# Kernel optimization log

Measured on AMD Instinct MI355X. Metric: run time of the kernel, lower is better.

The kernel has to match this reference:

```python
import jax, jax.numpy as jnp
import numpy as np

SH_C0 = 0.28209479177387814
SH_C1 = 0.4886025119029199
SH_C2 = (1.0925484305920792, -1.0925484305920792, 0.31539156525252005,
         -1.0925484305920792, 0.5462742152960396)
RADIUS = 0.006  # pyramid level k=0: 0.006 * 2**k


def eval_sh2(sh, dirs):
    # sh: [B, N, 16, 9], dirs: [N, 3] -> [B, N, 16]
    x = dirs[None, :, 0, None]
    y = dirs[None, :, 1, None]
    z = dirs[None, :, 2, None]
    xx, yy, zz = x * x, y * y, z * z
    res = (SH_C0 * sh[..., 0]
           - SH_C1 * y * sh[..., 1] + SH_C1 * z * sh[..., 2] - SH_C1 * x * sh[..., 3]
           + SH_C2[0] * (x * y) * sh[..., 4] + SH_C2[1] * (y * z) * sh[..., 5]
           + SH_C2[2] * (2.0 * zz - xx - yy) * sh[..., 6]
           + SH_C2[3] * (x * z) * sh[..., 7] + SH_C2[4] * (xx - yy) * sh[..., 8])
    return res


def setup_inputs() -> dict:
    key = jax.random.key(0)
    ks = jax.random.split(key, 9)
    P, F, H, W, C = 500000, 200000, 768, 768, 72
    features = jax.random.normal(ks[0], (P, C), jnp.float32)
    faces = jax.random.randint(ks[1], (F, 3), 0, P, jnp.int64)
    idx = jax.random.randint(ks[2], (2, H, W, 1), 0, P, jnp.int64)
    idx = jnp.where(jax.random.uniform(ks[3], (2, H, W, 1)) < 0.3, -1, idx)
    p2f = jax.random.randint(ks[4], (2, H, W, 1), 0, F, jnp.int64)
    p2f = jnp.where(jax.random.uniform(ks[5], (2, H, W, 1)) < 0.3, -1, p2f)
    dists = jax.random.uniform(ks[6], (2, H, W, 1), jnp.float32) * (RADIUS * RADIUS)
    bary = jax.random.uniform(ks[7], (2, H, W, 1, 3), jnp.float32)
    bary = bary / jnp.sum(bary, axis=-1, keepdims=True)
    rd = jax.random.normal(ks[8], (3, H, W), jnp.float32)
    rd = rd / jnp.linalg.norm(rd, axis=0, keepdims=True)
    return {"features": features, "frag1_dists": dists, "frag2_bary": bary,
            "ray_dirs": rd, "faces": faces, "frag1_idx": idx,
            "frag2_pix_to_face": p2f}


def reference(features, frag1_dists, frag2_bary, ray_dirs, faces, frag1_idx, frag2_pix_to_face):
    # frag1_idx / frag2_pix_to_face: [2, H, W, 1] (K=1), -1 == empty pixel
    H, W = frag1_idx.shape[1], frag1_idx.shape[2]
    m1 = frag1_idx >= 0
    m2 = frag2_pix_to_face >= 0
    final_mask = jnp.logical_or(m1, m2)            # [2, H, W, 1]
    weights = 1.0 - frag1_dists / (RADIUS * RADIUS)  # [2, H, W, 1]
    # point-rasterizer gather: features[idx] * mask * weights
    feat1 = features[jnp.maximum(frag1_idx, 0)]    # [2, H, W, 1, C]
    feat1 = feat1 * m1[..., None] * weights[..., None]
    feat1 = feat1[:, :, :, 0, :]                   # [2, H, W, C]
    # mesh-rasterizer barycentric interpolation (interpolate_face_attributes)
    tri = faces[jnp.maximum(frag2_pix_to_face, 0)]  # [2, H, W, 1, 3]
    colors = jnp.zeros_like(feat1)[:, :, :, None, :]
    for v in range(3):  # small fixed loop over triangle vertices
        colors = colors + frag2_bary[..., v:v + 1] * features[tri[..., v]]
    colors = colors * m2[..., None]
    colors = colors[:, :, :, 0, :]                 # [2, H, W, C]
    feat = jnp.concatenate([feat1, colors], axis=-1)  # [2, H, W, 144]
    # ray directions: flip along both image axes, then flatten to [H*W, 3]
    dirs = jnp.flip(ray_dirs, axis=(1, 2)).transpose(1, 2, 0).reshape(-1, 3)
    sh = feat.reshape(2, H * W, 16, 9)
    out = eval_sh2(sh, dirs).reshape(2, H, W, 16)
    out_feat_fg = out[0:1]
    out_feat_bg = out[1:2]
    final_mask_fg = final_mask[0:1]
    final_mask_bg = final_mask[1:2]
    return (out_feat_fg, out_feat_bg, final_mask_fg, final_mask_bg)
```

## Files before the change

kernel.cpp:

```cpp
#include <hip/hip_runtime.h>


constexpr float SH_C0 = 0.28209479177387814f;
constexpr float SH_C1 = 0.4886025119029199f;
constexpr float C20 =  1.0925484305920792f;
constexpr float C21 = -1.0925484305920792f;
constexpr float C22 =  0.31539156525252005f;
constexpr float C23 = -1.0925484305920792f;
constexpr float C24 =  0.5462742152960396f;
constexpr float INV_R2 = 1.0f / (0.006f * 0.006f);

__global__ __launch_bounds__(256) void net_tex_kernel8(
    const float* __restrict__ features,
    const float* __restrict__ dists,
    const float* __restrict__ bary,
    const float* __restrict__ rd,
    const int*  __restrict__ faces,
    const int*  __restrict__ f1idx,
    const int*  __restrict__ p2f,
    float* __restrict__ out,
    int HW, int N)
{
    int q = blockIdx.x * blockDim.x + threadIdx.x;
    int p = q >> 3;
    int r = q & 7;
    if (p >= N) return;
    int role = r >> 1;
    int half = r & 1;

    int s  = (p >= HW) ? 1 : 0;
    int hw = p - s * HW;

    float x = rd[HW   - 1 - hw];
    float y = rd[2*HW - 1 - hw];
    float z = rd[3*HW - 1 - hw];
    float xx = x*x, yy = y*y, zz = z*z;
    float c[9];
    c[0] = SH_C0;
    c[1] = -SH_C1 * y;
    c[2] =  SH_C1 * z;
    c[3] = -SH_C1 * x;
    c[4] = C20 * x * y;
    c[5] = C21 * y * z;
    c[6] = C22 * (2.0f*zz - xx - yy);
    c[7] = C23 * x * z;
    c[8] = C24 * (xx - yy);

    int   idx;
    float w;
    bool  valid;
    if (role == 0) {
        int i1 = f1idx[p];
        valid = (i1 >= 0);
        idx = valid ? i1 : 0;
        w = 1.0f - dists[p] * INV_R2;
    } else {
        int f2 = p2f[p];
        valid = (f2 >= 0);
        int fb = (valid ? f2 : 0) * 3;
        idx = faces[fb + (role - 1)];
        w = bary[(size_t)p * 3 + (role - 1)];
    }

    float d[4];
    #pragma unroll
    for (int j = 0; j < 4; j++) d[j] = 0.0f;

    if (valid) {
        const float4* row =
            (const float4*)(features + (size_t)idx * 72) + half * 9;
        #pragma unroll
        for (int ch = 0; ch < 9; ch++) {
            float4 v = row[ch];
            const int e = ch * 4;
            d[(e+0)/9] += c[(e+0)%9] * v.x;
            d[(e+1)/9] += c[(e+1)%9] * v.y;
            d[(e+2)/9] += c[(e+2)%9] * v.z;
            d[(e+3)/9] += c[(e+3)%9] * v.w;
        }
        #pragma unroll
        for (int j = 0; j < 4; j++) d[j] *= w;
    }

    float sum[4];
    #pragma unroll
    for (int j = 0; j < 4; j++) {
        float t = (role == 0) ? 0.0f : d[j];
        t += __shfl_xor(t, 2, 64);
        t += __shfl_xor(t, 4, 64);
        sum[j] = t;
    }

    unsigned long long bal = __ballot(valid);
    int lane = threadIdx.x & 63;
    bool any = ((bal >> (lane & ~7)) & 0xFFULL) != 0;

    float4* o = (float4*)(out + (size_t)p * 16);
    if (r == 0) {
        o[0] = make_float4(d[0], d[1], d[2], d[3]);
    } else if (r == 1) {
        o[1] = make_float4(d[0], d[1], d[2], d[3]);
    } else if (r == 2) {
        o[2] = make_float4(sum[0], sum[1], sum[2], sum[3]);
    } else if (r == 3) {
        o[3] = make_float4(sum[0], sum[1], sum[2], sum[3]);
    } else if (r == 4) {
        out[(size_t)2 * HW * 16 + p] = any ? 1.0f : 0.0f;
    }
}

extern "C" void kernel_launch(void* const* d_in, const int* in_sizes, int n_in,
                              void* d_out, int out_size, void* d_ws, size_t ws_size,
                              hipStream_t stream)
{
    const float* features = (const float*)d_in[0];
    const float* dists    = (const float*)d_in[1];
    const float* bary     = (const float*)d_in[2];
    const float* rd       = (const float*)d_in[3];
    const int*   faces    = (const int*)d_in[4];
    const int*   f1idx    = (const int*)d_in[5];
    const int*   p2f      = (const int*)d_in[6];
    float* out = (float*)d_out;

    int HW = in_sizes[1] / 2;
    int N  = 2 * HW;
    long long threads = (long long)N * 8;

    const int block = 256;
    const int grid  = (int)((threads + block - 1) / block);
    hipLaunchKernelGGL(net_tex_kernel8, dim3(grid), dim3(block), 0, stream,
                       features, dists, bary, rd, faces, f1idx, p2f, out, HW, N);
}
```

Baseline: 195.2 us.

## Stage gathered feature rows through LDS with cooperative float4 loads

Each block now handles 16 pixels. It first resolves the 64 row indices and weights into shared memory, then loads all gathered 72-float feature rows cooperatively into padded LDS rows before the SH evaluation reads them from LDS. The aim is to turn scattered per-thread 9-float4 reads into denser cooperative requests across the block, giving more memory-level parallelism. In exchange it adds two barriers, about 20KB of LDS per block (which limits occupancy), and smaller 128-thread blocks.

```diff
diff --git a/kernel.cpp b/kernel.cpp
--- a/kernel.cpp
+++ b/kernel.cpp
@@ -10,7 +10,12 @@
 constexpr float C24 =  0.5462742152960396f;
 constexpr float INV_R2 = 1.0f / (0.006f * 0.006f);
 
-__global__ __launch_bounds__(256) void net_tex_kernel8(
+constexpr int PPB     = 16;
+constexpr int THREADS = 128;
+constexpr int NROWS   = PPB * 4;
+constexpr int ROW_DW  = 76;
+
+__global__ __launch_bounds__(THREADS) void net_tex_stage(
     const float* __restrict__ features,
     const float* __restrict__ dists,
     const float* __restrict__ bary,
@@ -21,12 +26,53 @@
     float* __restrict__ out,
     int HW, int N)
 {
-    int q = blockIdx.x * blockDim.x + threadIdx.x;
-    int p = q >> 3;
-    int r = q & 7;
-    if (p >= N) return;
+    __shared__ float s_rows[NROWS * ROW_DW];
+    __shared__ int   s_idx[NROWS];
+    __shared__ float s_w[NROWS];
+
+    const int tid = threadIdx.x;
+    const int P0  = blockIdx.x * PPB;
+
+    if (tid < NROWS) {
+        int pix  = tid >> 2;
+        int role = tid & 3;
+        int p    = P0 + pix;
+        int idx  = -1;
+        float w  = 0.0f;
+        if (p < N) {
+            if (role == 0) {
+                int i1 = f1idx[p];
+                if (i1 >= 0) { idx = i1; w = 1.0f - dists[p] * INV_R2; }
+            } else {
+                int f2 = p2f[p];
+                if (f2 >= 0) {
+                    idx = faces[3 * f2 + (role - 1)];
+                    w   = bary[(size_t)3 * p + (role - 1)];
+                }
+            }
+        }
+        s_idx[tid] = idx;
+        s_w[tid]   = w;
+    }
+    __syncthreads();
+
+    for (int t = tid; t < NROWS * 18; t += THREADS) {
+        int rid = t / 18;
+        int m   = t - rid * 18;
+        int idx = s_idx[rid];
+        float4 v = make_float4(0.0f, 0.0f, 0.0f, 0.0f);
+        if (idx >= 0)
+            v = ((const float4*)(features + (size_t)idx * 72))[m];
+        *(float4*)(s_rows + rid * ROW_DW + m * 4) = v;
+    }
+    __syncthreads();
+
+    int pix  = tid >> 3;
+    int r    = tid & 7;
     int role = r >> 1;
     int half = r & 1;
+    int p    = P0 + pix;
+    if (p >= N) return;
 
     int s  = (p >= HW) ? 1 : 0;
     int hw = p - s * HW;
@@ -46,41 +92,27 @@
     c[7] = C23 * x * z;
     c[8] = C24 * (xx - yy);
 
-    int   idx;
-    float w;
-    bool  valid;
-    if (role == 0) {
-        int i1 = f1idx[p];
-        valid = (i1 >= 0);
-        idx = valid ? i1 : 0;
-        w = 1.0f - dists[p] * INV_R2;
-    } else {
-        int f2 = p2f[p];
-        valid = (f2 >= 0);
-        int fb = (valid ? f2 : 0) * 3;
-        idx = faces[fb + (role - 1)];
-        w = bary[(size_t)p * 3 + (role - 1)];
-    }
+    int   slot  = pix * 4 + role;
+    bool  valid = s_idx[slot] >= 0;
+    float w     = s_w[slot];
+
+    const float4* row = (const float4*)(s_rows + slot * ROW_DW) + half * 9;
 
     float d[4];
     #pragma unroll
     for (int j = 0; j < 4; j++) d[j] = 0.0f;
 
-    if (valid) {
-        const float4* row =
-            (const float4*)(features + (size_t)idx * 72) + half * 9;
-        #pragma unroll
-        for (int ch = 0; ch < 9; ch++) {
-            float4 v = row[ch];
-            const int e = ch * 4;
-            d[(e+0)/9] += c[(e+0)%9] * v.x;
-            d[(e+1)/9] += c[(e+1)%9] * v.y;
-            d[(e+2)/9] += c[(e+2)%9] * v.z;
-            d[(e+3)/9] += c[(e+3)%9] * v.w;
-        }
-        #pragma unroll
-        for (int j = 0; j < 4; j++) d[j] *= w;
+    #pragma unroll
+    for (int ch = 0; ch < 9; ch++) {
+        float4 v = row[ch];
+        const int e = ch * 4;
+        d[(e+0)/9] += c[(e+0)%9] * v.x;
+        d[(e+1)/9] += c[(e+1)%9] * v.y;
+        d[(e+2)/9] += c[(e+2)%9] * v.z;
+        d[(e+3)/9] += c[(e+3)%9] * v.w;
     }
+    #pragma unroll
+    for (int j = 0; j < 4; j++) d[j] *= w;
 
     float sum[4];
     #pragma unroll
@@ -92,7 +124,7 @@
     }
 
     unsigned long long bal = __ballot(valid);
-    int lane = threadIdx.x & 63;
+    int lane = tid & 63;
     bool any = ((bal >> (lane & ~7)) & 0xFFULL) != 0;
 
     float4* o = (float4*)(out + (size_t)p * 16);
@@ -124,10 +156,8 @@
 
     int HW = in_sizes[1] / 2;
     int N  = 2 * HW;
-    long long threads = (long long)N * 8;
 
-    const int block = 256;
-    const int grid  = (int)((threads + block - 1) / block);
-    hipLaunchKernelGGL(net_tex_kernel8, dim3(grid), dim3(block), 0, stream,
+    int grid = (N + PPB - 1) / PPB;
+    hipLaunchKernelGGL(net_tex_stage, dim3(grid), dim3(THREADS), 0, stream,
                        features, dists, bary, rd, faces, f1idx, p2f, out, HW, N);
 }
```

Result: slower. 254.5 us (+30.4%).
